# Kernel tuning notes

Measured on AMD Instinct MI355X. Metric: run time of the kernel, lower is better.

Reference implementation:

```python
import jax, jax.numpy as jnp
import numpy as np

TEMPERATURE = 0.1  # from __init__ temperature
NEG_INF = -1e30


def setup_inputs() -> dict:
    key = jax.random.key(0)
    k1, k2, k3, k4, k5 = jax.random.split(key, 5)
    B, D = 8192, 128
    return {
        "zis": jax.random.normal(k1, (B, D), dtype=jnp.float32),
        "zjs": jax.random.normal(k2, (B, D), dtype=jnp.float32),
        "ilabels": jax.random.randint(k3, (B,), 0, 100, dtype=jnp.int64),
        "jlabels": jax.random.randint(k4, (B,), 0, 100, dtype=jnp.int64),
        "weights": jax.random.uniform(k5, (B,), dtype=jnp.float32),
        "idx": 0,
    }


def reference(zis, zjs, ilabels, jlabels, weights, idx):
    B = zjs.shape[0]
    # forward F.normalize + cosine_matrix's normalize is idempotent -> single L2 normalize
    zi = zis / jnp.linalg.norm(zis, axis=1, keepdims=True)
    zj = zjs / jnp.linalg.norm(zjs, axis=1, keepdims=True)
    # similarity_matrix = 1 - (1 - zj @ zi^T); rows indexed by zjs
    logits = (zj @ zi.T) / TEMPERATURE  # [B, B]
    # labels[i, j] = (ilabels[j] == jlabels[i])
    labels = ilabels[None, :] == jlabels[:, None]  # [B, B] bool
    neg_mask = ~labels  # 'zeros' columns per row
    rows = jnp.arange(B)
    pos_idx = idx + rows  # class_level=False: ones = idx + i, size = 1
    pos = logits[rows, pos_idx]  # [B]
    # CrossEntropy over cat([pos, logits[i, zeros]]) at label 0:
    # loss_i = logsumexp([pos_i, neg_row_i]) - pos_i (numerically stable)
    neg_max = jnp.max(jnp.where(neg_mask, logits, NEG_INF), axis=1)
    m = jnp.maximum(pos, neg_max)  # [B]
    denom = jnp.exp(pos - m) + jnp.sum(
        jnp.where(neg_mask, jnp.exp(logits - m[:, None]), 0.0), axis=1
    )
    loss = m + jnp.log(denom) - pos  # [B]
    # size==1 path: loss*w / w (faithful to torch weighted sum / weight.sum())
    w = weights[pos_idx]
    loss = (loss * w) / w
    return jnp.sum(loss) / B
```

## Files before the change

### kernel.cpp

```cpp
#include <hip/hip_runtime.h>


#define BB 8192
#define DD 128
#define CP 256
#define RSL 512
#define NGR 16

typedef __attribute__((ext_vector_type(8))) short short8;
typedef __attribute__((ext_vector_type(4))) float floatx4;

#define GLOBAL_AS __attribute__((address_space(1)))
#define LDS_AS    __attribute__((address_space(3)))

#define L2E10 14.4269504088896340f

static __device__ __forceinline__ float wave_sum(float v) {
#pragma unroll
    for (int off = 32; off > 0; off >>= 1) v += __shfl_xor(v, off, 64);
    return v;
}

static __device__ __forceinline__ unsigned short f2bf(float f) {
    unsigned int u = __float_as_uint(f);
    return (unsigned short)((u + 0x7FFFu + ((u >> 16) & 1u)) >> 16);
}

__global__ __launch_bounds__(256) void prep_kernel(
    const float* __restrict__ zis, const float* __restrict__ zjs,
    unsigned short* __restrict__ Zib, unsigned short* __restrict__ Zjb,
    float* __restrict__ rni, float* __restrict__ rnj,
    float* __restrict__ denom, float* __restrict__ out, int nout)
{
    if (threadIdx.x < 2) denom[blockIdx.x * 2 + threadIdx.x] = 0.0f;
    if (blockIdx.x == 0 && (int)threadIdx.x < nout) out[threadIdx.x] = 0.0f;

    int wave = threadIdx.x >> 6, lane = threadIdx.x & 63;
    int row = blockIdx.x * 4 + wave;
    const float* src; unsigned short* dst; float* rn; int r;
    if (row < BB) { src = zis; dst = Zib; rn = rni; r = row; }
    else          { src = zjs; dst = Zjb; rn = rnj; r = row - BB; }
    float2 u = *(const float2*)(src + (size_t)r * DD + lane * 2);
    float s = wave_sum(u.x * u.x + u.y * u.y);
    float sc = 1.0f / sqrtf(s);
    if (lane == 0) rn[r] = sc;
    ushort2 o; o.x = f2bf(u.x * sc); o.y = f2bf(u.y * sc);
    *(ushort2*)(dst + (size_t)r * DD + lane * 2) = o;
}

__global__ __launch_bounds__(512, 2) void panel_kernel(
    const unsigned short* __restrict__ Zjb,
    const unsigned short* __restrict__ Zib,
    const int* __restrict__ ilab, const int* __restrict__ jlab,
    float* __restrict__ denom)
{
    __shared__ __align__(16) unsigned short Bp[CP * DD];
    __shared__ int Il[CP];

    int tid  = threadIdx.x;
    int lane = tid & 63, wave = tid >> 6;
    int quad = lane >> 4, l15 = lane & 15;
    int c0    = blockIdx.y * CP;
    int rbase = blockIdx.x * RSL;

    {
        int nl = wave * 4 + quad;
        int s  = l15 ^ (nl & 15);
        const unsigned short* gp0 = Zib + (size_t)(c0 + nl) * DD + s * 8;
#pragma unroll
        for (int u = 0; u < 8; ++u) {
            const unsigned short* gp = gp0 + (size_t)u * 32 * DD;
            unsigned short* lp = &Bp[(u * 8 + wave) * 512];
            __builtin_amdgcn_global_load_lds((const GLOBAL_AS void*)gp,
                                             (LDS_AS void*)lp, 16, 0, 0);
        }
    }
    if (tid < CP) Il[tid] = ilab[c0 + tid];
    asm volatile("s_waitcnt vmcnt(0) lgkmcnt(0)" ::: "memory");
    __builtin_amdgcn_s_barrier();

#pragma unroll
    for (int c = 0; c < 2; ++c) {
        int r0 = rbase + wave * 64 + c * 32;

        short8 af[2][4];
#pragma unroll
        for (int mt = 0; mt < 2; ++mt)
#pragma unroll
            for (int ks = 0; ks < 4; ++ks)
                af[mt][ks] = *(const short8*)(Zjb
                    + (size_t)(r0 + mt * 16 + l15) * DD + ks * 32 + quad * 8);

        int jrv[8];
#pragma unroll
        for (int mt = 0; mt < 2; ++mt)
#pragma unroll
            for (int r = 0; r < 4; ++r)
                jrv[mt * 4 + r] = jlab[r0 + mt * 16 + quad * 4 + r];

        float rs[2][4];
#pragma unroll
        for (int mt = 0; mt < 2; ++mt)
#pragma unroll
            for (int r = 0; r < 4; ++r) rs[mt][r] = 0.0f;

        floatx4 acc[2];
        int iln = Il[l15];

        __builtin_amdgcn_s_setprio(1);
#pragma unroll
        for (int g = 0; g < NGR; ++g) {
            const unsigned short* rb = &Bp[(g * 16 + l15) * DD];
            short8 b[4];
#pragma unroll
            for (int ks = 0; ks < 4; ++ks)
                b[ks] = *(const short8*)(rb + (((ks * 4 + quad) ^ l15) * 8));
            floatx4 zz = (floatx4){0.f, 0.f, 0.f, 0.f};
            acc[0] = __builtin_amdgcn_mfma_f32_16x16x32_bf16(af[0][0], b[0], zz, 0, 0, 0);
            acc[1] = __builtin_amdgcn_mfma_f32_16x16x32_bf16(af[1][0], b[0], zz, 0, 0, 0);
#pragma unroll
            for (int ks = 1; ks < 4; ++ks) {
                acc[0] = __builtin_amdgcn_mfma_f32_16x16x32_bf16(af[0][ks], b[ks], acc[0], 0, 0, 0);
                acc[1] = __builtin_amdgcn_mfma_f32_16x16x32_bf16(af[1][ks], b[ks], acc[1], 0, 0, 0);
            }
            int ilc = iln;
            if (g + 1 < NGR) iln = Il[(g + 1) * 16 + l15];
#pragma unroll
            for (int mt = 0; mt < 2; ++mt)
#pragma unroll
                for (int r = 0; r < 4; ++r) {
                    float e = __builtin_amdgcn_exp2f(
                        fmaf(acc[mt][r], L2E10, -L2E10));
                    rs[mt][r] += (ilc != jrv[mt * 4 + r]) ? e : 0.0f;
                }
        }
        __builtin_amdgcn_s_setprio(0);

#pragma unroll
        for (int mt = 0; mt < 2; ++mt)
#pragma unroll
            for (int r = 0; r < 4; ++r) {
                float v = rs[mt][r];
                v += __shfl_xor(v, 1, 64);
                v += __shfl_xor(v, 2, 64);
                v += __shfl_xor(v, 4, 64);
                v += __shfl_xor(v, 8, 64);
                if (l15 == 0)
                    atomicAdd(&denom[r0 + mt * 16 + quad * 4 + r], v);
            }
    }
}

__global__ __launch_bounds__(256) void posfinal_kernel(
    const float* __restrict__ zis, const float* __restrict__ zjs,
    const float* __restrict__ rni, const float* __restrict__ rnj,
    const float* __restrict__ denom, const float* __restrict__ wts,
    const int* __restrict__ idxp, float* __restrict__ out)
{
    int wave = threadIdx.x >> 6, lane = threadIdx.x & 63;
    int idx = idxp[0];
    float ll = 0.0f;
#pragma unroll
    for (int t = 0; t < 4; ++t) {
        int i = blockIdx.x * 16 + wave * 4 + t;
        int j = idx + i;
        float2 a  = *(const float2*)(zjs + (size_t)i * DD + lane * 2);
        float2 b2 = *(const float2*)(zis + (size_t)j * DD + lane * 2);
        float s = wave_sum(a.x * b2.x + a.y * b2.y);
        if (lane == 0) {
            float p = s * rni[j] * rnj[i] * 10.0f;
            float l = 10.0f + logf(__expf(p - 10.0f) + denom[i]) - p;
            float w = wts[j];
            ll += (l * w) / w;
        }
    }
    __shared__ float part[4];
    if (lane == 0) part[wave] = ll;
    __syncthreads();
    if (threadIdx.x == 0)
        atomicAdd(out, (part[0] + part[1] + part[2] + part[3]) * (1.0f / BB));
}

extern "C" void kernel_launch(void* const* d_in, const int* in_sizes, int n_in,
                              void* d_out, int out_size, void* d_ws, size_t ws_size,
                              hipStream_t stream) {
    const float* zis = (const float*)d_in[0];
    const float* zjs = (const float*)d_in[1];
    const int* ilab = (const int*)d_in[2];
    const int* jlab = (const int*)d_in[3];
    const float* wts = (const float*)d_in[4];
    const int* idxp = (const int*)d_in[5];
    float* out = (float*)d_out;

    float* rni   = (float*)d_ws;
    float* rnj   = rni + BB;
    float* denom = rnj + BB;
    unsigned short* Zib = (unsigned short*)(denom + BB);
    unsigned short* Zjb = Zib + (size_t)BB * DD;

    prep_kernel<<<2 * BB / 4, 256, 0, stream>>>(
        zis, zjs, Zib, Zjb, rni, rnj, denom, out, out_size);
    panel_kernel<<<dim3(BB / RSL, BB / CP), 512, 0, stream>>>(
        Zjb, Zib, ilab, jlab, denom);
    posfinal_kernel<<<BB / 16, 256, 0, stream>>>(
        zis, zjs, rni, rnj, denom, wts, idxp, out);
}
```

Before: 110.7 us.

## Fuse panel and positive-loss kernels with per-wave double-buffered column streaming

Merges the similarity panel kernel and the final loss kernel into one launch. Each block owns 32 rows and its 16 waves each stream 512 columns of Zib through a per-wave double-buffered LDS slice using async global-to-LDS loads. Row sums stay in shared memory, which removes the global denom buffer, its zeroing and the global atomics. In exchange, each block reloads all of Zib (256 blocks each read the full matrix) and copies all 8192 labels into LDS, so L2 traffic rises and each block carries more setup work.

After: 254.8 us. 130% more time.

```diff
diff --git a/kernel.cpp b/kernel.cpp
--- a/kernel.cpp
+++ b/kernel.cpp
@@ -3,9 +3,9 @@
 
 #define BB 8192
 #define DD 128
-#define CP 256
-#define RSL 512
-#define NGR 16
+#define RPB 32
+#define CPW 512
+#define NCH 32
 
 typedef __attribute__((ext_vector_type(8))) short short8;
 typedef __attribute__((ext_vector_type(4))) float floatx4;
@@ -30,9 +30,8 @@
     const float* __restrict__ zis, const float* __restrict__ zjs,
     unsigned short* __restrict__ Zib, unsigned short* __restrict__ Zjb,
     float* __restrict__ rni, float* __restrict__ rnj,
-    float* __restrict__ denom, float* __restrict__ out, int nout)
+    float* __restrict__ out, int nout)
 {
-    if (threadIdx.x < 2) denom[blockIdx.x * 2 + threadIdx.x] = 0.0f;
     if (blockIdx.x == 0 && (int)threadIdx.x < nout) out[threadIdx.x] = 0.0f;
 
     int wave = threadIdx.x >> 6, lane = threadIdx.x & 63;
@@ -48,137 +47,154 @@
     *(ushort2*)(dst + (size_t)r * DD + lane * 2) = o;
 }
 
-__global__ __launch_bounds__(512, 2) void panel_kernel(
+__global__ __launch_bounds__(1024, 4) void fused_kernel(
     const unsigned short* __restrict__ Zjb,
     const unsigned short* __restrict__ Zib,
     const int* __restrict__ ilab, const int* __restrict__ jlab,
-    float* __restrict__ denom)
+    const float* __restrict__ zis, const float* __restrict__ zjs,
+    const float* __restrict__ rni, const float* __restrict__ rnj,
+    const float* __restrict__ wts, const int* __restrict__ idxp,
+    float* __restrict__ out)
 {
-    __shared__ __align__(16) unsigned short Bp[CP * DD];
-    __shared__ int Il[CP];
+    __shared__ __align__(16) unsigned short Bp[16 * 4096];
+    __shared__ unsigned short Il2[BB];
+    __shared__ float rowsum[RPB];
+    __shared__ float part[16];
 
     int tid  = threadIdx.x;
     int lane = tid & 63, wave = tid >> 6;
     int quad = lane >> 4, l15 = lane & 15;
-    int c0    = blockIdx.y * CP;
-    int rbase = blockIdx.x * RSL;
-
-    {
-        int nl = wave * 4 + quad;
-        int s  = l15 ^ (nl & 15);
-        const unsigned short* gp0 = Zib + (size_t)(c0 + nl) * DD + s * 8;
-#pragma unroll
-        for (int u = 0; u < 8; ++u) {
-            const unsigned short* gp = gp0 + (size_t)u * 32 * DD;
-            unsigned short* lp = &Bp[(u * 8 + wave) * 512];
-            __builtin_amdgcn_global_load_lds((const GLOBAL_AS void*)gp,
-                                             (LDS_AS void*)lp, 16, 0, 0);
+    int r0  = blockIdx.x * RPB;
+    int cw0 = wave * CPW;
+
+#pragma unroll
+    for (int k = 0; k < BB / 1024; ++k)
+        Il2[k * 1024 + tid] = (unsigned short)ilab[k * 1024 + tid];
+    if (tid < RPB) rowsum[tid] = 0.0f;
+    __syncthreads();
+
+    short8 af[2][4];
+#pragma unroll
+    for (int mt = 0; mt < 2; ++mt)
+#pragma unroll
+        for (int ks = 0; ks < 4; ++ks)
+            af[mt][ks] = *(const short8*)(Zjb
+                + (size_t)(r0 + mt * 16 + l15) * DD + ks * 32 + quad * 8);
+
+    int jrv[8];
+#pragma unroll
+    for (int mt = 0; mt < 2; ++mt)
+#pragma unroll
+        for (int r = 0; r < 4; ++r)
+            jrv[mt * 4 + r] = jlab[r0 + mt * 16 + quad * 4 + r];
+
+    unsigned short* wsl = &Bp[wave * 4096];
+    const unsigned short* rb0 = wsl + l15 * 128 + (((0 + quad) ^ l15) * 8);
+    const unsigned short* rb1 = wsl + l15 * 128 + (((4 + quad) ^ l15) * 8);
+    const unsigned short* rb2 = wsl + l15 * 128 + (((8 + quad) ^ l15) * 8);
+    const unsigned short* rb3 = wsl + l15 * 128 + (((12 + quad) ^ l15) * 8);
+
+    const unsigned short* g0 = Zib + (size_t)(cw0 + 0 + quad) * DD + ((l15 ^ (0 + quad)) * 8);
+    const unsigned short* g1 = Zib + (size_t)(cw0 + 4 + quad) * DD + ((l15 ^ (4 + quad)) * 8);
+    const unsigned short* g2 = Zib + (size_t)(cw0 + 8 + quad) * DD + ((l15 ^ (8 + quad)) * 8);
+    const unsigned short* g3 = Zib + (size_t)(cw0 + 12 + quad) * DD + ((l15 ^ (12 + quad)) * 8);
+
+#define STG(g) do {                                                         \
+        unsigned short* lb = wsl + ((g) & 1) * 2048;                        \
+        __builtin_amdgcn_global_load_lds((const GLOBAL_AS void*)(g0 + (g) * 2048), \
+                                         (LDS_AS void*)(lb + 0 * 512), 16, 0, 0);  \
+        __builtin_amdgcn_global_load_lds((const GLOBAL_AS void*)(g1 + (g) * 2048), \
+                                         (LDS_AS void*)(lb + 1 * 512), 16, 0, 0);  \
+        __builtin_amdgcn_global_load_lds((const GLOBAL_AS void*)(g2 + (g) * 2048), \
+                                         (LDS_AS void*)(lb + 2 * 512), 16, 0, 0);  \
+        __builtin_amdgcn_global_load_lds((const GLOBAL_AS void*)(g3 + (g) * 2048), \
+                                         (LDS_AS void*)(lb + 3 * 512), 16, 0, 0);  \
+    } while (0)
+
+    float rs[2][4];
+#pragma unroll
+    for (int mt = 0; mt < 2; ++mt)
+#pragma unroll
+        for (int r = 0; r < 4; ++r) rs[mt][r] = 0.0f;
+
+    STG(0);
+    STG(1);
+
+    __builtin_amdgcn_s_setprio(1);
+#pragma unroll
+    for (int g = 0; g < NCH; ++g) {
+        if (g < NCH - 1) asm volatile("s_waitcnt vmcnt(4)" ::: "memory");
+        else             asm volatile("s_waitcnt vmcnt(0)" ::: "memory");
+        const int P = (g & 1) * 2048;
+        short8 b0 = *(const short8*)(rb0 + P);
+        short8 b1 = *(const short8*)(rb1 + P);
+        short8 b2 = *(const short8*)(rb2 + P);
+        short8 b3 = *(const short8*)(rb3 + P);
+        int ilg = (int)Il2[cw0 + g * 16 + l15];
+        asm volatile("s_waitcnt lgkmcnt(0)" ::: "memory");
+        if (g + 2 < NCH) STG(g + 2);
+
+        floatx4 zz = (floatx4){0.f, 0.f, 0.f, 0.f};
+        floatx4 acc0, acc1;
+        acc0 = __builtin_amdgcn_mfma_f32_16x16x32_bf16(af[0][0], b0, zz, 0, 0, 0);
+        acc1 = __builtin_amdgcn_mfma_f32_16x16x32_bf16(af[1][0], b0, zz, 0, 0, 0);
+        acc0 = __builtin_amdgcn_mfma_f32_16x16x32_bf16(af[0][1], b1, acc0, 0, 0, 0);
+        acc1 = __builtin_amdgcn_mfma_f32_16x16x32_bf16(af[1][1], b1, acc1, 0, 0, 0);
+        acc0 = __builtin_amdgcn_mfma_f32_16x16x32_bf16(af[0][2], b2, acc0, 0, 0, 0);
+        acc1 = __builtin_amdgcn_mfma_f32_16x16x32_bf16(af[1][2], b2, acc1, 0, 0, 0);
+        acc0 = __builtin_amdgcn_mfma_f32_16x16x32_bf16(af[0][3], b3, acc0, 0, 0, 0);
+        acc1 = __builtin_amdgcn_mfma_f32_16x16x32_bf16(af[1][3], b3, acc1, 0, 0, 0);
+
+#pragma unroll
+        for (int r = 0; r < 4; ++r) {
+            float e0 = __builtin_amdgcn_exp2f(fmaf(acc0[r], L2E10, -L2E10));
+            rs[0][r] += (ilg != jrv[r]) ? e0 : 0.0f;
+            float e1 = __builtin_amdgcn_exp2f(fmaf(acc1[r], L2E10, -L2E10));
+            rs[1][r] += (ilg != jrv[4 + r]) ? e1 : 0.0f;
         }
     }
-    if (tid < CP) Il[tid] = ilab[c0 + tid];
-    asm volatile("s_waitcnt vmcnt(0) lgkmcnt(0)" ::: "memory");
-    __builtin_amdgcn_s_barrier();
-
-#pragma unroll
-    for (int c = 0; c < 2; ++c) {
-        int r0 = rbase + wave * 64 + c * 32;
-
-        short8 af[2][4];
-#pragma unroll
-        for (int mt = 0; mt < 2; ++mt)
-#pragma unroll
-            for (int ks = 0; ks < 4; ++ks)
-                af[mt][ks] = *(const short8*)(Zjb
-                    + (size_t)(r0 + mt * 16 + l15) * DD + ks * 32 + quad * 8);
-
-        int jrv[8];
-#pragma unroll
-        for (int mt = 0; mt < 2; ++mt)
-#pragma unroll
-            for (int r = 0; r < 4; ++r)
-                jrv[mt * 4 + r] = jlab[r0 + mt * 16 + quad * 4 + r];
-
-        float rs[2][4];
-#pragma unroll
-        for (int mt = 0; mt < 2; ++mt)
-#pragma unroll
-            for (int r = 0; r < 4; ++r) rs[mt][r] = 0.0f;
-
-        floatx4 acc[2];
-        int iln = Il[l15];
-
-        __builtin_amdgcn_s_setprio(1);
-#pragma unroll
-        for (int g = 0; g < NGR; ++g) {
-            const unsigned short* rb = &Bp[(g * 16 + l15) * DD];
-            short8 b[4];
-#pragma unroll
-            for (int ks = 0; ks < 4; ++ks)
-                b[ks] = *(const short8*)(rb + (((ks * 4 + quad) ^ l15) * 8));
-            floatx4 zz = (floatx4){0.f, 0.f, 0.f, 0.f};
-            acc[0] = __builtin_amdgcn_mfma_f32_16x16x32_bf16(af[0][0], b[0], zz, 0, 0, 0);
-            acc[1] = __builtin_amdgcn_mfma_f32_16x16x32_bf16(af[1][0], b[0], zz, 0, 0, 0);
-#pragma unroll
-            for (int ks = 1; ks < 4; ++ks) {
-                acc[0] = __builtin_amdgcn_mfma_f32_16x16x32_bf16(af[0][ks], b[ks], acc[0], 0, 0, 0);
-                acc[1] = __builtin_amdgcn_mfma_f32_16x16x32_bf16(af[1][ks], b[ks], acc[1], 0, 0, 0);
-            }
-            int ilc = iln;
-            if (g + 1 < NGR) iln = Il[(g + 1) * 16 + l15];
-#pragma unroll
-            for (int mt = 0; mt < 2; ++mt)
-#pragma unroll
-                for (int r = 0; r < 4; ++r) {
-                    float e = __builtin_amdgcn_exp2f(
-                        fmaf(acc[mt][r], L2E10, -L2E10));
-                    rs[mt][r] += (ilc != jrv[mt * 4 + r]) ? e : 0.0f;
-                }
+    __builtin_amdgcn_s_setprio(0);
+#undef STG
+
+#pragma unroll
+    for (int mt = 0; mt < 2; ++mt)
+#pragma unroll
+        for (int r = 0; r < 4; ++r) {
+            float v = rs[mt][r];
+            v += __shfl_xor(v, 1, 64);
+            v += __shfl_xor(v, 2, 64);
+            v += __shfl_xor(v, 4, 64);
+            v += __shfl_xor(v, 8, 64);
+            if (l15 == 0)
+                atomicAdd(&rowsum[mt * 16 + quad * 4 + r], v);
         }
-        __builtin_amdgcn_s_setprio(0);
-
-#pragma unroll
-        for (int mt = 0; mt < 2; ++mt)
-#pragma unroll
-            for (int r = 0; r < 4; ++r) {
-                float v = rs[mt][r];
-                v += __shfl_xor(v, 1, 64);
-                v += __shfl_xor(v, 2, 64);
-                v += __shfl_xor(v, 4, 64);
-                v += __shfl_xor(v, 8, 64);
-                if (l15 == 0)
-                    atomicAdd(&denom[r0 + mt * 16 + quad * 4 + r], v);
-            }
-    }
-}
-
-__global__ __launch_bounds__(256) void posfinal_kernel(
-    const float* __restrict__ zis, const float* __restrict__ zjs,
-    const float* __restrict__ rni, const float* __restrict__ rnj,
-    const float* __restrict__ denom, const float* __restrict__ wts,
-    const int* __restrict__ idxp, float* __restrict__ out)
-{
-    int wave = threadIdx.x >> 6, lane = threadIdx.x & 63;
-    int idx = idxp[0];
+    __syncthreads();
+
+    int idx2 = idxp[0];
     float ll = 0.0f;
 #pragma unroll
-    for (int t = 0; t < 4; ++t) {
-        int i = blockIdx.x * 16 + wave * 4 + t;
-        int j = idx + i;
+    for (int t = 0; t < 2; ++t) {
+        int irl = wave * 2 + t;
+        int i = r0 + irl;
+        int j = idx2 + i;
         float2 a  = *(const float2*)(zjs + (size_t)i * DD + lane * 2);
         float2 b2 = *(const float2*)(zis + (size_t)j * DD + lane * 2);
         float s = wave_sum(a.x * b2.x + a.y * b2.y);
         if (lane == 0) {
             float p = s * rni[j] * rnj[i] * 10.0f;
-            float l = 10.0f + logf(__expf(p - 10.0f) + denom[i]) - p;
+            float l = 10.0f + logf(__expf(p - 10.0f) + rowsum[irl]) - p;
             float w = wts[j];
             ll += (l * w) / w;
         }
     }
-    __shared__ float part[4];
     if (lane == 0) part[wave] = ll;
     __syncthreads();
-    if (threadIdx.x == 0)
-        atomicAdd(out, (part[0] + part[1] + part[2] + part[3]) * (1.0f / BB));
+    if (tid == 0) {
+        float sum = 0.0f;
+#pragma unroll
+        for (int q = 0; q < 16; ++q) sum += part[q];
+        atomicAdd(out, sum * (1.0f / BB));
+    }
 }
 
 extern "C" void kernel_launch(void* const* d_in, const int* in_sizes, int n_in,
@@ -194,14 +210,11 @@
 
     float* rni   = (float*)d_ws;
     float* rnj   = rni + BB;
-    float* denom = rnj + BB;
-    unsigned short* Zib = (unsigned short*)(denom + BB);
+    unsigned short* Zib = (unsigned short*)(rnj + BB);
     unsigned short* Zjb = Zib + (size_t)BB * DD;
 
     prep_kernel<<<2 * BB / 4, 256, 0, stream>>>(
-        zis, zjs, Zib, Zjb, rni, rnj, denom, out, out_size);
-    panel_kernel<<<dim3(BB / RSL, BB / CP), 512, 0, stream>>>(
-        Zjb, Zib, ilab, jlab, denom);
-    posfinal_kernel<<<BB / 16, 256, 0, stream>>>(
-        zis, zjs, rni, rnj, denom, wts, idxp, out);
-}
+        zis, zjs, Zib, Zjb, rni, rnj, out, out_size);
+    fused_kernel<<<BB / RPB, 1024, 0, stream>>>(
+        Zjb, Zib, ilab, jlab, zis, zjs, rni, rnj, wts, idxp, out);
+}
```
